# Kernel optimization log

Hardware: AMD Instinct MI355X
Metric: run time of the kernel (lower is better)

Reference implementation:

```python
import jax, jax.numpy as jnp
import numpy as np

# dims
B, N, L = 8, 128, 512          # batch, n_vars, context_window
PL, ST = 16, 8                  # patch_len, stride
PN = (L - PL) // ST + 1         # patch_num = 63
DM, H, DFF, NL = 128, 16, 256, 2
DK = DM // H
DG, MP, BETA = 8, 3, 0.05       # d_gcn, mp_layers, propbeta
TW = 96                         # target_window


def setup_inputs() -> dict:
    key = jax.random.key(0)
    ks = iter(jax.random.split(key, 64))
    def nrm(shape, s=0.02):
        return jax.random.normal(next(ks), shape, jnp.float32) * s
    inp = {
        "x": jax.random.normal(next(ks), (B, N, L), jnp.float32),
        "adj_logits": jax.random.normal(next(ks), (B, L, N, N), jnp.float32),
        # DGCN params
        "dgcn_start_w": nrm((1, DG)), "dgcn_start_b": jnp.zeros((DG,), jnp.float32),
        "dgcn_mlp_w": nrm(((MP + 1) * DG, 1)), "dgcn_mlp_b": jnp.zeros((1,), jnp.float32),
        # patch embedding + positional
        "W_P": nrm((PL, DM)), "b_P": jnp.zeros((DM,), jnp.float32), "W_pos": nrm((PN, DM)),
        # encoder layers (stacked over NL)
        "Wq": nrm((NL, DM, DM)), "bq": jnp.zeros((NL, DM), jnp.float32),
        "Wk": nrm((NL, DM, DM)), "bk": jnp.zeros((NL, DM), jnp.float32),
        "Wv": nrm((NL, DM, DM)), "bv": jnp.zeros((NL, DM), jnp.float32),
        "Wo": nrm((NL, DM, DM)), "bo": jnp.zeros((NL, DM), jnp.float32),
        "scale": jnp.full((NL,), DK ** -0.5, jnp.float32),
        "bn1_g": jnp.ones((NL, DM), jnp.float32), "bn1_b": jnp.zeros((NL, DM), jnp.float32),
        "ff_w1": nrm((NL, DM, DFF)), "ff_b1": jnp.zeros((NL, DFF), jnp.float32),
        "ff_w2": nrm((NL, DFF, DM)), "ff_b2": jnp.zeros((NL, DM), jnp.float32),
        "bn2_g": jnp.ones((NL, DM), jnp.float32), "bn2_b": jnp.zeros((NL, DM), jnp.float32),
        # head
        "head_w": nrm((DM * PN, TW)), "head_b": jnp.zeros((TW,), jnp.float32),
    }
    return inp


def _bn(x, g, b):
    # BatchNorm1d in training mode over (batch, seq) per feature channel
    mu = x.mean(axis=(0, 1))
    var = x.var(axis=(0, 1))
    return (x - mu) * jax.lax.rsqrt(var + 1e-5) * g + b


def reference(x, adj_logits, dgcn_start_w, dgcn_start_b, dgcn_mlp_w, dgcn_mlp_b,
              W_P, b_P, W_pos, Wq, bq, Wk, bk, Wv, bv, Wo, bo, scale,
              bn1_g, bn1_b, ff_w1, ff_b1, ff_w2, ff_b2, bn2_g, bn2_b,
              head_w, head_b):
    # ---- DGCN: multi-hop diffusion over variables, per time step ----
    x4 = x[..., None]                                   # [b,n,s,1]
    A = jax.nn.softmax(adj_logits, axis=2)              # [b,s,n,m], normalized over source n
    a = jnp.transpose(A, (0, 2, 3, 1))                  # [b,n,m,s]
    h = x4 @ dgcn_start_w + dgcn_start_b                # [b,n,s,d_gcn]
    outs = [h]
    for _ in range(MP):
        h = BETA * x4 + (1.0 - BETA) * jnp.einsum('bnsc,bnms->bmsc', h, a)
        outs.append(h)
    y = (jnp.concatenate(outs, axis=-1) @ dgcn_mlp_w + dgcn_mlp_b)[..., 0]  # [b,n,s]
    # ---- patching ----
    win = jnp.arange(PN)[:, None] * ST + jnp.arange(PL)[None, :]
    z = y[:, :, win]                                    # [b,n,pn,pl]
    # ---- TSTiEncoder (channel independent) ----
    src = (z @ W_P + b_P).reshape(B * N, PN, DM) + W_pos
    prev = None
    for l in range(NL):
        q = (src @ Wq[l] + bq[l]).reshape(-1, PN, H, DK).transpose(0, 2, 1, 3)
        k = (src @ Wk[l] + bk[l]).reshape(-1, PN, H, DK).transpose(0, 2, 1, 3)
        v = (src @ Wv[l] + bv[l]).reshape(-1, PN, H, DK).transpose(0, 2, 1, 3)
        scores = jnp.einsum('bhqd,bhkd->bhqk', q, k) * scale[l]
        if prev is not None:
            scores = scores + prev                      # residual attention
        w = jax.nn.softmax(scores, axis=-1)
        o = jnp.einsum('bhqk,bhkd->bhqd', w, v).transpose(0, 2, 1, 3).reshape(-1, PN, DM)
        src = _bn(src + (o @ Wo[l] + bo[l]), bn1_g[l], bn1_b[l])
        ff = jax.nn.gelu(src @ ff_w1[l] + ff_b1[l], approximate=False) @ ff_w2[l] + ff_b2[l]
        src = _bn(src + ff, bn2_g[l], bn2_b[l])
        prev = scores
    # ---- Flatten_Head ----
    enc = src.reshape(B, N, PN, DM).transpose(0, 1, 3, 2).reshape(B, N, DM * PN)
    return enc @ head_w + head_b                        # [b, n_vars, target_window]
```

## Files before the change

### kernel.cpp

```cpp
#include <hip/hip_runtime.h>
#include <hip/hip_bf16.h>
#include <math.h>

#define RM 64512

typedef short short8 __attribute__((ext_vector_type(8)));
typedef float f32x4 __attribute__((ext_vector_type(4)));
typedef unsigned short ushort4v __attribute__((ext_vector_type(4)));
typedef unsigned short ushort8v __attribute__((ext_vector_type(8)));

__device__ __forceinline__ float gelu_f(float v) {
    return 0.5f * v * (1.0f + erff(v * 0.70710678118654752f));
}
__device__ __forceinline__ float b2f(unsigned short u) {
    unsigned int x = ((unsigned int)u) << 16;
    return __builtin_bit_cast(float, x);
}
__device__ __forceinline__ unsigned short f2b(float f) {
    __hip_bfloat16 h = __float2bfloat16(f);
    return __builtin_bit_cast(unsigned short, h);
}

__global__ __launch_bounds__(256) void dgcn_kernel(
    const float* __restrict__ x, const float* __restrict__ adj,
    const float* __restrict__ sw, const float* __restrict__ sb,
    const float* __restrict__ mw, const float* __restrict__ mb,
    float* __restrict__ y,
    const float* __restrict__ Wq, const float* __restrict__ Wk, const float* __restrict__ Wv,
    const float* __restrict__ Wo, const float* __restrict__ fw1, const float* __restrict__ fw2,
    const float* __restrict__ bq, const float* __restrict__ bk, const float* __restrict__ bv,
    unsigned short* __restrict__ WB, float* __restrict__ bcat)
{
    if (blockIdx.x >= 4096) {
        const int wb = blockIdx.x - 4096;
        const int id = wb / 64, bx = wb % 64;
        const int l = id / 6, mat = id % 6;
        const float* src; int K, N; size_t off = (size_t)l * 131072;
        switch (mat) {
            case 0: src = Wq  + l*16384; K = 128; N = 128; off += 0;      break;
            case 1: src = Wk  + l*16384; K = 128; N = 128; off += 16384;  break;
            case 2: src = Wv  + l*16384; K = 128; N = 128; off += 32768;  break;
            case 3: src = Wo  + l*16384; K = 128; N = 128; off += 49152;  break;
            case 4: src = fw1 + l*32768; K = 128; N = 256; off += 65536;  break;
            default:src = fw2 + l*32768; K = 256; N = 128; off += 98304;  break;
        }
        const int total = K * N;
        const int ksh = (K == 256) ? 8 : 7;
        for (int idx = bx*256 + threadIdx.x; idx < total; idx += 64*256) {
            int n = idx >> ksh, k = idx & (K - 1);
            WB[off + idx] = f2b(src[(size_t)k*N + n]);
        }
        if (id == 0 && bx == 0) {
            for (int idx = threadIdx.x; idx < 768; idx += 256) {
                int ll = idx / 384, j = idx % 384;
                float vv;
                if (j < 128)      vv = bq[ll*128 + j];
                else if (j < 256) vv = bk[ll*128 + j - 128];
                else              vv = bv[ll*128 + j - 256];
                bcat[idx] = vv;
            }
        }
        return;
    }
    __shared__ __align__(16) unsigned short ET[128*128];
    __shared__ __align__(16) unsigned short hT[16*128];
    __shared__ float red[256];
    __shared__ float iv[128];
    __shared__ float xc[128];
    __shared__ float yac[128];
    const int bid = blockIdx.x;
    const int b = bid >> 9, s = bid & 511;
    const int t = threadIdx.x;
    const int lane = t & 63, wid = t >> 6;
    const float* ap = adj + (size_t)bid * 16384;

    if (t < 128) xc[t] = x[((size_t)b*128 + t)*512 + s];

    {
        const int m = t & 127, ng = t >> 7;
        float sm = 0.f;
        for (int p = 0; p < 16; ++p) {
            const int n0 = p*8 + ng*4;
            float e0 = __expf(ap[(size_t)(n0+0)*128 + m]);
            float e1 = __expf(ap[(size_t)(n0+1)*128 + m]);
            float e2 = __expf(ap[(size_t)(n0+2)*128 + m]);
            float e3 = __expf(ap[(size_t)(n0+3)*128 + m]);
            sm += e0 + e1 + e2 + e3;
            ushort4v u4; u4[0]=f2b(e0); u4[1]=f2b(e1); u4[2]=f2b(e2); u4[3]=f2b(e3);
            *(ushort4v*)((char*)ET + m*256 + (((n0>>3) ^ (m & 15))*16) + (n0 & 7)*2) = u4;
        }
        red[ng*128 + m] = sm;
        *(ushort4v*)&hT[8*128 + t*4] = (ushort4v){0,0,0,0};
    }
    __syncthreads();
    if (t < 128) iv[t] = 1.f / (red[t] + red[128 + t]);
    if (t < 128) {
        const int m = t;
        const float xm = xc[m];
        float yp = 0.f;
        #pragma unroll
        for (int c = 0; c < 8; ++c) {
            float h = xm*sw[c] + sb[c];
            yp += h*mw[c];
            *(unsigned short*)((char*)hT + c*256 + ((((m>>3) ^ c))*16) + (m & 7)*2) = f2b(h);
        }
        yac[m] = yp;
    }
    __syncthreads();

    const int rl = lane & 15, kh = lane >> 4;
    short8 af[2][4];
    float xr[2][4], ivr[2][4];
    #pragma unroll
    for (int ti = 0; ti < 2; ++ti) {
        const int mrow = (wid*2 + ti)*16 + rl;
        #pragma unroll
        for (int ks = 0; ks < 4; ++ks) {
            const int ch = (ks*4 + kh) ^ (mrow & 15);
            af[ti][ks] = *(const short8*)((const char*)ET + mrow*256 + ch*16);
        }
        #pragma unroll
        for (int r = 0; r < 4; ++r) {
            const int m = (wid*2 + ti)*16 + kh*4 + r;
            xr[ti][r]  = 0.05f * xc[m];
            ivr[ti][r] = 0.95f * iv[m];
        }
    }
    float yl[2][4] = {};
    #pragma unroll
    for (int step = 1; step <= 3; ++step) {
        short8 bfr[4];
        #pragma unroll
        for (int ks = 0; ks < 4; ++ks) {
            const int ch = (ks*4 + kh) ^ rl;
            bfr[ks] = *(const short8*)((const char*)hT + rl*256 + ch*16);
        }
        f32x4 acc[2] = {};
        #pragma unroll
        for (int ti = 0; ti < 2; ++ti)
            #pragma unroll
            for (int ks = 0; ks < 4; ++ks)
                acc[ti] = __builtin_amdgcn_mfma_f32_16x16x32_bf16(af[ti][ks], bfr[ks], acc[ti], 0, 0, 0);
        __syncthreads();
        const float mwc = (rl < 8) ? mw[step*8 + rl] : 0.f;
        #pragma unroll
        for (int ti = 0; ti < 2; ++ti) {
            const int m0 = (wid*2 + ti)*16 + kh*4;
            ushort4v hw4;
            float hnew[4];
            #pragma unroll
            for (int r = 0; r < 4; ++r) {
                float v = xr[ti][r] + ivr[ti][r]*acc[ti][r];
                hnew[r] = v;
                hw4[r] = f2b(v);
            }
            *(ushort4v*)((char*)hT + rl*256 + (((m0>>3) ^ rl)*16) + (m0 & 7)*2) = hw4;
            #pragma unroll
            for (int r = 0; r < 4; ++r) {
                float vv = hnew[r]*mwc;
                vv += __shfl_xor(vv, 1);
                vv += __shfl_xor(vv, 2);
                vv += __shfl_xor(vv, 4);
                vv += __shfl_xor(vv, 8);
                yl[ti][r] += vv;
            }
        }
        __syncthreads();
    }
    if (rl == 0) {
        #pragma unroll
        for (int ti = 0; ti < 2; ++ti)
            #pragma unroll
            for (int r = 0; r < 4; ++r)
                yac[(wid*2 + ti)*16 + kh*4 + r] += yl[ti][r];
    }
    __syncthreads();
    if (t < 128) y[((size_t)b*128 + t)*512 + s] = yac[t] + mb[0];
}

__global__ __launch_bounds__(256) void patch_kernel(
    const float* __restrict__ y, const float* __restrict__ Wp, const float* __restrict__ bp,
    const float* __restrict__ Wpos, unsigned short* __restrict__ srcb)
{
    __shared__ float ys[512];
    __shared__ float wps[16*128];
    const int bn = blockIdx.x;
    const int t = threadIdx.x;
    ys[t]       = y[(size_t)bn*512 + t];
    ys[t + 256] = y[(size_t)bn*512 + t + 256];
    #pragma unroll
    for (int r = 0; r < 8; ++r) wps[t + r*256] = Wp[t + r*256];
    __syncthreads();
    for (int cu = t; cu < 1008; cu += 256) {
        int p = cu >> 4, d0 = (cu & 15) * 8;
        float o[8];
        #pragma unroll
        for (int j = 0; j < 8; ++j) o[j] = bp[d0+j] + Wpos[p*128 + d0 + j];
        #pragma unroll
        for (int tt = 0; tt < 16; ++tt) {
            float a = ys[p*8 + tt];
            #pragma unroll
            for (int j = 0; j < 8; ++j) o[j] += a * wps[tt*128 + d0 + j];
        }
        size_t row = (size_t)bn*63 + p;
        ushort8v u;
        #pragma unroll
        for (int j = 0; j < 8; ++j) u[j] = f2b(o[j]);
        *(ushort8v*)&srcb[row*128 + d0] = u;
    }
}

template<int ACT, int OM, int RESMODE, bool STATS, bool AHM, int NB, int KK>
__global__ __launch_bounds__(256) void mgemm(
    const unsigned short* __restrict__ A, const unsigned short* __restrict__ WB,
    const float* __restrict__ bias, const unsigned short* __restrict__ Rsd,
    const float* __restrict__ snR,
    unsigned short* __restrict__ Cb,
    float* __restrict__ part)
{
    constexpr int NTOT = NB * 128;
    constexpr int kch = KK >> 3;
    constexpr int KT = KK >> 7;
    __shared__ __align__(16) unsigned short AsL[64*128];
    __shared__ __align__(16) unsigned short BsL[128*128];
    __shared__ float sred[4][16][8], qred[4][16][8];
    const int t = threadIdx.x;
    const int lane = t & 63, wid = t >> 6;
    const int wr = wid >> 1, wc = wid & 1;
    const int m0 = blockIdx.x * 64;
    const int kh = lane >> 4, rl = lane & 15;
    const int rq = lane >> 4;
    float sj[8] = {}, qj[8] = {};

    for (int ib = 0; ib < NB; ++ib) {
        f32x4 acc[2][4] = {};
        for (int kt = 0; kt < KT; ++kt) {
            if (ib == 0 || KT > 1) {
                #pragma unroll
                for (int i = 0; i < 4; ++i) {
                    int cid = i*256 + t;
                    const unsigned short* ga;
                    if constexpr (AHM) {
                        int hd2 = cid >> 6, row = cid & 63;
                        ga = A + ((size_t)hd2*RM + (m0+row))*8;
                    } else {
                        int row = cid >> 4, c = cid & 15;
                        int c_g = c ^ (row & 7);
                        ga = A + ((size_t)(m0+row)*kch + kt*16 + c_g)*8;
                    }
                    __builtin_amdgcn_global_load_lds((const unsigned int*)ga,
                        (unsigned int*)&AsL[(i*256 + wid*64)*8], 16, 0, 0);
                }
            }
            #pragma unroll
            for (int i = 0; i < 8; ++i) {
                int cid = i*256 + t;
                int nr = cid >> 4, c = cid & 15;
                const unsigned short* gb = WB + (size_t)ib*128*KK
                    + ((size_t)nr*kch + kt*16 + (c ^ (nr & 7)))*8;
                __builtin_amdgcn_global_load_lds((const unsigned int*)gb,
                    (unsigned int*)&BsL[(i*256 + wid*64)*8], 16, 0, 0);
            }
            __syncthreads();
            #pragma unroll
            for (int ks = 0; ks < 4; ++ks) {
                const int cA = ks*4 + kh;
                short8 af[2], bfr[4];
                #pragma unroll
                for (int i = 0; i < 2; ++i) {
                    int row = wr*32 + i*16 + rl;
                    if constexpr (AHM) af[i] = *(const short8*)&AsL[(cA*64 + row)*8];
                    else               af[i] = *(const short8*)&AsL[row*128 + ((cA ^ (row & 7))*8)];
                }
                #pragma unroll
                for (int j = 0; j < 4; ++j) {
                    int cn = wc*64 + j*16 + rl;
                    bfr[j] = *(const short8*)&BsL[cn*128 + ((cA ^ (cn & 7))*8)];
                }
                #pragma unroll
                for (int i = 0; i < 2; ++i)
                    #pragma unroll
                    for (int j = 0; j < 4; ++j)
                        acc[i][j] = __builtin_amdgcn_mfma_f32_16x16x32_bf16(af[i], bfr[j], acc[i][j], 0, 0, 0);
            }
            __syncthreads();
        }
        #pragma unroll
        for (int j = 0; j < 4; ++j) {
            const int col_l = wc*64 + j*16 + rl;
            const float bs = bias[ib*128 + col_l];
            const int chunk = col_l >> 3, bo2 = (col_l & 7) << 1;
            #pragma unroll
            for (int i = 0; i < 2; ++i) {
                #pragma unroll
                for (int r = 0; r < 4; ++r) {
                    const int row_l = wr*32 + i*16 + rq*4 + r;
                    float v = acc[i][j][r] + bs;
                    if constexpr (ACT == 1) v = gelu_f(v);
                    *(unsigned short*)((char*)BsL + row_l*256 + ((chunk ^ (row_l & 15))<<4) + bo2) = f2b(v);
                }
            }
        }
        __syncthreads();
        if constexpr (OM == 1) {
            #pragma unroll
            for (int it = 0; it < 4; ++it) {
                int cid = it*256 + t;
                int row_l = cid & 63, hd_l = cid >> 6;
                ushort8v u = *(const ushort8v*)((const char*)BsL + row_l*256 + ((hd_l ^ (row_l & 15))<<4));
                *(ushort8v*)&Cb[(((size_t)(ib*16 + hd_l))*RM + m0 + row_l)*8] = u;
            }
        } else {
            #pragma unroll
            for (int it = 0; it < 4; ++it) {
                const int row_l = it*16 + (t >> 4), c = t & 15;
                ushort8v u = *(const ushort8v*)((const char*)BsL + row_l*256 + ((c ^ (row_l & 15))<<4));
                const size_t gbase = (size_t)(m0 + row_l)*NTOT + ib*128 + c*8;
                ushort8v rs = {};
                if constexpr (RESMODE != 0) rs = *(const ushort8v*)&Rsd[gbase];
                ushort8v o8;
                #pragma unroll
                for (int jj = 0; jj < 8; ++jj) {
                    float v = b2f(u[jj]);
                    if constexpr (RESMODE == 1) v += b2f(rs[jj]);
                    if constexpr (RESMODE == 2) v += b2f(rs[jj])*snR[c*8+jj] + snR[128 + c*8 + jj];
                    if constexpr (STATS) { sj[jj] += v; qj[jj] += v*v; }
                    o8[jj] = f2b(v);
                }
                *(ushort8v*)&Cb[gbase] = o8;
            }
        }
        __syncthreads();
    }
    if constexpr (STATS) {
        #pragma unroll
        for (int jj = 0; jj < 8; ++jj) {
            sj[jj] += __shfl_xor(sj[jj], 16); qj[jj] += __shfl_xor(qj[jj], 16);
            sj[jj] += __shfl_xor(sj[jj], 32); qj[jj] += __shfl_xor(qj[jj], 32);
        }
        if ((lane >> 4) == 0) {
            #pragma unroll
            for (int jj = 0; jj < 8; ++jj) {
                sred[wid][lane][jj] = sj[jj];
                qred[wid][lane][jj] = qj[jj];
            }
        }
        __syncthreads();
        if (t < 128) {
            const int c2 = t >> 3, jj = t & 7;
            float s = sred[0][c2][jj] + sred[1][c2][jj] + sred[2][c2][jj] + sred[3][c2][jj];
            float q = qred[0][c2][jj] + qred[1][c2][jj] + qred[2][c2][jj] + qred[3][c2][jj];
            part[(size_t)blockIdx.x*256 + t]       = s;
            part[(size_t)blockIdx.x*256 + 128 + t] = q;
        }
    }
}

__global__ __launch_bounds__(256) void ffused(
    const unsigned short* __restrict__ A, const unsigned short* __restrict__ W1,
    const float* __restrict__ b1, const unsigned short* __restrict__ W2,
    const float* __restrict__ b2, const unsigned short* __restrict__ Rsd,
    const float* __restrict__ snR,
    unsigned short* __restrict__ Cb, float* __restrict__ part)
{
    __shared__ __align__(16) char smem[81920];
    unsigned short* AsL = (unsigned short*)smem;
    unsigned short* BsL = (unsigned short*)(smem + 16384);
    unsigned short* G   = (unsigned short*)(smem + 49152);
    float* sred = (float*)(smem + 49152);
    float* qred = sred + 512;
    const int t = threadIdx.x;
    const int lane = t & 63, wid = t >> 6;
    const int wr = wid >> 1, wc = wid & 1;
    const int m0 = blockIdx.x * 64;
    const int kh = lane >> 4, rl = lane & 15;
    const int rq = lane >> 4;

    #pragma unroll
    for (int i = 0; i < 4; ++i) {
        int cid = i*256 + t;
        int row = cid >> 4, c = cid & 15;
        const unsigned short* ga = A + ((size_t)(m0+row)*16 + (c ^ (row & 7)))*8;
        __builtin_amdgcn_global_load_lds((const unsigned int*)ga,
            (unsigned int*)&AsL[(i*256 + wid*64)*8], 16, 0, 0);
    }
    #pragma unroll
    for (int i = 0; i < 8; ++i) {
        int cid = i*256 + t;
        int nr = cid >> 4, c = cid & 15;
        const unsigned short* gb = W1 + ((size_t)nr*16 + (c ^ (nr & 7)))*8;
        __builtin_amdgcn_global_load_lds((const unsigned int*)gb,
            (unsigned int*)&BsL[(i*256 + wid*64)*8], 16, 0, 0);
    }
    __syncthreads();
    for (int ib = 0; ib < 2; ++ib) {
        f32x4 acc[2][4] = {};
        #pragma unroll
        for (int ks = 0; ks < 4; ++ks) {
            const int cA = ks*4 + kh;
            short8 af[2], bfr[4];
            #pragma unroll
            for (int i = 0; i < 2; ++i) {
                int row = wr*32 + i*16 + rl;
                af[i] = *(const short8*)&AsL[row*128 + ((cA ^ (row & 7))*8)];
            }
            #pragma unroll
            for (int j = 0; j < 4; ++j) {
                int cn = wc*64 + j*16 + rl;
                bfr[j] = *(const short8*)&BsL[cn*128 + ((cA ^ (cn & 7))*8)];
            }
            #pragma unroll
            for (int i = 0; i < 2; ++i)
                #pragma unroll
                for (int j = 0; j < 4; ++j)
                    acc[i][j] = __builtin_amdgcn_mfma_f32_16x16x32_bf16(af[i], bfr[j], acc[i][j], 0, 0, 0);
        }
        __syncthreads();
        if (ib == 0) {
            #pragma unroll
            for (int i = 0; i < 8; ++i) {
                int cid = i*256 + t;
                int nr = cid >> 4, c = cid & 15;
                const unsigned short* gb = W1 + ((size_t)(128+nr)*16 + (c ^ (nr & 7)))*8;
                __builtin_amdgcn_global_load_lds((const unsigned int*)gb,
                    (unsigned int*)&BsL[(i*256 + wid*64)*8], 16, 0, 0);
            }
        }
        #pragma unroll
        for (int j = 0; j < 4; ++j) {
            const int col_l = wc*64 + j*16 + rl;
            const int colg = ib*128 + col_l;
            const float bs = b1[colg];
            const int cg = colg >> 3, bo2 = (colg & 7) << 1;
            #pragma unroll
            for (int i = 0; i < 2; ++i) {
                #pragma unroll
                for (int r = 0; r < 4; ++r) {
                    const int row_l = wr*32 + i*16 + rq*4 + r;
                    float v = gelu_f(acc[i][j][r] + bs);
                    *(unsigned short*)((char*)G + row_l*512 + (((cg ^ (row_l & 15)))<<4) + bo2) = f2b(v);
                }
            }
        }
        __syncthreads();
    }
    f32x4 acc2[2][4] = {};
    for (int kt = 0; kt < 2; ++kt) {
        #pragma unroll
        for (int i = 0; i < 8; ++i) {
            int cid = i*256 + t;
            int nr = cid >> 4, c = cid & 15;
            const unsigned short* gb = W2 + ((size_t)nr*32 + kt*16 + (c ^ (nr & 7)))*8;
            __builtin_amdgcn_global_load_lds((const unsigned int*)gb,
                (unsigned int*)&BsL[(i*256 + wid*64)*8], 16, 0, 0);
        }
        __syncthreads();
        #pragma unroll
        for (int ks = 0; ks < 4; ++ks) {
            const int cA = ks*4 + kh;
            short8 af[2], bfr[4];
            #pragma unroll
            for (int i = 0; i < 2; ++i) {
                int row = wr*32 + i*16 + rl;
                af[i] = *(const short8*)((const char*)G + row*512 + ((((kt*16 + cA) ^ (row & 15)))<<4));
            }
            #pragma unroll
            for (int j = 0; j < 4; ++j) {
                int cn = wc*64 + j*16 + rl;
                bfr[j] = *(const short8*)&BsL[cn*128 + ((cA ^ (cn & 7))*8)];
            }
            #pragma unroll
            for (int i = 0; i < 2; ++i)
                #pragma unroll
                for (int j = 0; j < 4; ++j)
                    acc2[i][j] = __builtin_amdgcn_mfma_f32_16x16x32_bf16(af[i], bfr[j], acc2[i][j], 0, 0, 0);
        }
        __syncthreads();
    }
    #pragma unroll
    for (int j = 0; j < 4; ++j) {
        const int col_l = wc*64 + j*16 + rl;
        const float bs = b2[col_l];
        const int chunk = col_l >> 3, bo2 = (col_l & 7) << 1;
        #pragma unroll
        for (int i = 0; i < 2; ++i) {
            #pragma unroll
            for (int r = 0; r < 4; ++r) {
                const int row_l = wr*32 + i*16 + rq*4 + r;
                *(unsigned short*)((char*)AsL + row_l*256 + ((chunk ^ (row_l & 15))<<4) + bo2)
                    = f2b(acc2[i][j][r] + bs);
            }
        }
    }
    __syncthreads();
    float sj[8] = {}, qj[8] = {};
    #pragma unroll
    for (int it = 0; it < 4; ++it) {
        const int row_l = it*16 + (t >> 4), c = t & 15;
        ushort8v u = *(const ushort8v*)((const char*)AsL + row_l*256 + ((c ^ (row_l & 15))<<4));
        const size_t gbase = (size_t)(m0 + row_l)*128 + c*8;
        ushort8v rs = *(const ushort8v*)&Rsd[gbase];
        ushort8v o8;
        #pragma unroll
        for (int jj = 0; jj < 8; ++jj) {
            float v = b2f(u[jj]) + b2f(rs[jj])*snR[c*8+jj] + snR[128 + c*8 + jj];
            sj[jj] += v; qj[jj] += v*v;
            o8[jj] = f2b(v);
        }
        *(ushort8v*)&Cb[gbase] = o8;
    }
    #pragma unroll
    for (int jj = 0; jj < 8; ++jj) {
        sj[jj] += __shfl_xor(sj[jj], 16); qj[jj] += __shfl_xor(qj[jj], 16);
        sj[jj] += __shfl_xor(sj[jj], 32); qj[jj] += __shfl_xor(qj[jj], 32);
    }
    if ((lane >> 4) == 0) {
        #pragma unroll
        for (int jj = 0; jj < 8; ++jj) {
            sred[wid*128 + lane*8 + jj] = sj[jj];
            qred[wid*128 + lane*8 + jj] = qj[jj];
        }
    }
    __syncthreads();
    if (t < 128) {
        const int c2 = t >> 3, jj = t & 7;
        float s = sred[0*128 + c2*8 + jj] + sred[1*128 + c2*8 + jj]
                + sred[2*128 + c2*8 + jj] + sred[3*128 + c2*8 + jj];
        float q = qred[0*128 + c2*8 + jj] + qred[1*128 + c2*8 + jj]
                + qred[2*128 + c2*8 + jj] + qred[3*128 + c2*8 + jj];
        part[(size_t)blockIdx.x*256 + t]       = s;
        part[(size_t)blockIdx.x*256 + 128 + t] = q;
    }
}

__global__ __launch_bounds__(256) void bnred(const float* __restrict__ part,
    const float* __restrict__ g, const float* __restrict__ b, float* __restrict__ sn)
{
    const int c = blockIdx.x, t = threadIdx.x;
    float s = 0.f, q = 0.f;
    for (int bid = t; bid < 1008; bid += 256) {
        s += part[(size_t)bid*256 + c];
        q += part[(size_t)bid*256 + 128 + c];
    }
    __shared__ float ls[256], lq[256];
    ls[t] = s; lq[t] = q;
    __syncthreads();
    for (int o = 128; o > 0; o >>= 1) {
        if (t < o) { ls[t] += ls[t+o]; lq[t] += lq[t+o]; }
        __syncthreads();
    }
    if (t == 0) {
        const float invM = 1.f / (float)RM;
        float mean = ls[0] * invM;
        float var  = fmaxf(lq[0]*invM - mean*mean, 0.f);
        float sc = g[c] * rsqrtf(var + 1e-5f);
        sn[c]       = sc;
        sn[128 + c] = b[c] - mean*sc;
    }
}

__global__ __launch_bounds__(256) void wfold(const unsigned short* __restrict__ WBs,
    const float* __restrict__ sn, const float* __restrict__ bsrc,
    unsigned short* __restrict__ WBd, float* __restrict__ bdst)
{
    const int t = threadIdx.x, wv = t >> 6, lane = t & 63;
    const int n = blockIdx.x*4 + wv;
    float w1 = b2f(WBs[(size_t)n*128 + lane]);
    float w2 = b2f(WBs[(size_t)n*128 + 64 + lane]);
    WBd[(size_t)n*128 + lane]      = f2b(sn[lane]*w1);
    WBd[(size_t)n*128 + 64 + lane] = f2b(sn[64+lane]*w2);
    float bacc = sn[128+lane]*w1 + sn[192+lane]*w2;
    #pragma unroll
    for (int msk = 1; msk < 64; msk <<= 1) bacc += __shfl_xor(bacc, msk);
    if (lane == 0) bdst[n] = bsrc[n] + bacc;
}

template<int L>
__global__ __launch_bounds__(256) void attn_kernel(
    const unsigned short* __restrict__ qkv, const unsigned short* __restrict__ qkvP,
    const float* __restrict__ scale, unsigned short* __restrict__ ob)
{
    __shared__ float ks[4][504], vs[4][504], k0s[4][504];
    const int bn = blockIdx.x;
    const int t = threadIdx.x, wid = t >> 6, lane = t & 63;
    const int hd = blockIdx.y*4 + wid;
    const size_t rbase = (size_t)hd*RM + (size_t)bn*63;
    float qr[8] = {}, q0r[8] = {};
    if (lane < 63) {
        ushort8v ku = *(const ushort8v*)&qkv[((size_t)16*RM*8) + (rbase + lane)*8];
        ushort8v vu = *(const ushort8v*)&qkv[((size_t)32*RM*8) + (rbase + lane)*8];
        #pragma unroll
        for (int d = 0; d < 8; ++d) { ks[wid][lane*8+d] = b2f(ku[d]); vs[wid][lane*8+d] = b2f(vu[d]); }
        ushort8v qu = *(const ushort8v*)&qkv[(rbase + lane)*8];
        #pragma unroll
        for (int d = 0; d < 8; ++d) qr[d] = b2f(qu[d]);
        if constexpr (L > 0) {
            ushort8v k0u = *(const ushort8v*)&qkvP[((size_t)16*RM*8) + (rbase + lane)*8];
            #pragma unroll
            for (int d = 0; d < 8; ++d) k0s[wid][lane*8+d] = b2f(k0u[d]);
            ushort8v q0u = *(const ushort8v*)&qkvP[(rbase + lane)*8];
            #pragma unroll
            for (int d = 0; d < 8; ++d) q0r[d] = b2f(q0u[d]);
        }
    }
    __syncthreads();
    if (lane >= 63) return;
    const float scl  = scale[L];
    const float scl0 = (L > 0) ? scale[0] : 0.f;
    float sum = 0.f;
    float oa[8] = {};
    for (int j = 0; j < 63; ++j) {
        float s = 0.f;
        #pragma unroll
        for (int d = 0; d < 8; ++d) s += qr[d]*ks[wid][j*8+d];
        s *= scl;
        if constexpr (L > 0) {
            float s0 = 0.f;
            #pragma unroll
            for (int d = 0; d < 8; ++d) s0 += q0r[d]*k0s[wid][j*8+d];
            s += scl0 * s0;
        }
        float p = __expf(s);
        sum += p;
        #pragma unroll
        for (int d = 0; d < 8; ++d) oa[d] += p*vs[wid][j*8+d];
    }
    float inv = 1.f / sum;
    ushort8v u;
    #pragma unroll
    for (int d = 0; d < 8; ++d) u[d] = f2b(oa[d]*inv);
    *(ushort8v*)&ob[((size_t)hd*RM + (size_t)bn*63 + lane)*8] = u;
}

__global__ __launch_bounds__(256) void hprep(
    const float* __restrict__ hw, const float* __restrict__ hb,
    const float* __restrict__ sn,
    unsigned short* __restrict__ hwTf, float* __restrict__ hbf)
{
    const int t = threadIdx.x;
    if (blockIdx.x < 63) {
        const int p = blockIdx.x;
        for (int idx = t; idx < 16384; idx += 256) {
            int n = idx >> 7, d = idx & 127;
            unsigned short w = 0;
            if (n < 96) w = f2b(sn[d] * hw[(size_t)(d*63 + p)*96 + n]);
            hwTf[((size_t)p*128 + n)*128 + d] = w;
        }
    } else {
        const int n = blockIdx.x - 63;
        float acc = 0.f;
        for (int k = t; k < 8064; k += 256) {
            int d = (int)(((unsigned)k * 33289u) >> 21);
            acc += sn[128 + d] * hw[(size_t)k*96 + n];
        }
        __shared__ float ls[256];
        ls[t] = acc;
        __syncthreads();
        for (int o = 128; o > 0; o >>= 1) { if (t < o) ls[t] += ls[t+o]; __syncthreads(); }
        if (t == 0) hbf[n] = hb[n] + ls[0];
    }
}

__global__ __launch_bounds__(256) void mhead(
    const unsigned short* __restrict__ A, const unsigned short* __restrict__ BW,
    float* __restrict__ part)
{
    __shared__ __align__(16) unsigned short AsL[128*128];
    __shared__ __align__(16) unsigned short BsL[128*128];
    const int t = threadIdx.x;
    const int lane = t & 63, wid = t >> 6;
    const int wr = wid >> 1, wc = wid & 1;
    const int m0 = blockIdx.x * 128;
    const int p  = blockIdx.y;
    #pragma unroll
    for (int i = 0; i < 8; ++i) {
        int cid = i*256 + t;
        int row = cid >> 4, c = cid & 15;
        const unsigned short* ga = A + ((size_t)(m0+row)*63 + p)*128 + ((c ^ (row & 7))*8);
        __builtin_amdgcn_global_load_lds((const unsigned int*)ga,
            (unsigned int*)&AsL[(i*256 + wid*64)*8], 16, 0, 0);
    }
    #pragma unroll
    for (int i = 0; i < 8; ++i) {
        int cid = i*256 + t;
        int nr = cid >> 4, c = cid & 15;
        const unsigned short* gb = BW + ((size_t)p*128 + nr)*128 + ((c ^ (nr & 7))*8);
        __builtin_amdgcn_global_load_lds((const unsigned int*)gb,
            (unsigned int*)&BsL[(i*256 + wid*64)*8], 16, 0, 0);
    }
    __syncthreads();
    const int kh = lane >> 4, rl = lane & 15;
    f32x4 acc[4][3] = {};
    #pragma unroll
    for (int kq = 0; kq < 4; ++kq) {
        const int cA = kq*4 + kh;
        short8 af[4], bfr[3];
        #pragma unroll
        for (int i = 0; i < 4; ++i) {
            int row = wr*64 + i*16 + rl;
            af[i] = *(const short8*)&AsL[row*128 + ((cA ^ (row & 7))*8)];
        }
        #pragma unroll
        for (int j = 0; j < 3; ++j) {
            int cn = wc*48 + j*16 + rl;
            bfr[j] = *(const short8*)&BsL[cn*128 + ((cA ^ (cn & 7))*8)];
        }
        #pragma unroll
        for (int i = 0; i < 4; ++i)
            #pragma unroll
            for (int j = 0; j < 3; ++j)
                acc[i][j] = __builtin_amdgcn_mfma_f32_16x16x32_bf16(af[i], bfr[j], acc[i][j], 0, 0, 0);
    }
    const int rl2 = lane & 15, rq = lane >> 4;
    #pragma unroll
    for (int j = 0; j < 3; ++j) {
        const int col = wc*48 + j*16 + rl2;
        #pragma unroll
        for (int i = 0; i < 4; ++i) {
            const int rbase = m0 + wr*64 + i*16 + rq*4;
            #pragma unroll
            for (int r = 0; r < 4; ++r)
                part[((size_t)p*1024 + rbase + r)*96 + col] = acc[i][j][r];
        }
    }
}

__global__ __launch_bounds__(256) void head_reduce(const float* __restrict__ part,
    const float* __restrict__ hbf, float* __restrict__ out)
{
    int idx = blockIdx.x*256 + threadIdx.x;
    float s = hbf[idx % 96];
    #pragma unroll
    for (int blk = 0; blk < 63; ++blk) s += part[(size_t)blk*98304 + idx];
    out[idx] = s;
}

extern "C" void kernel_launch(void* const* d_in, const int* in_sizes, int n_in,
                              void* d_out, int out_size, void* d_ws, size_t ws_size,
                              hipStream_t stream) {
    const float* x    = (const float*)d_in[0];
    const float* adj  = (const float*)d_in[1];
    const float* sw   = (const float*)d_in[2];
    const float* sb   = (const float*)d_in[3];
    const float* mw   = (const float*)d_in[4];
    const float* mb   = (const float*)d_in[5];
    const float* Wp   = (const float*)d_in[6];
    const float* bp   = (const float*)d_in[7];
    const float* Wpos = (const float*)d_in[8];
    const float* Wq   = (const float*)d_in[9];
    const float* bq   = (const float*)d_in[10];
    const float* Wk   = (const float*)d_in[11];
    const float* bk   = (const float*)d_in[12];
    const float* Wv   = (const float*)d_in[13];
    const float* bv   = (const float*)d_in[14];
    const float* Wo   = (const float*)d_in[15];
    const float* bo   = (const float*)d_in[16];
    const float* scale= (const float*)d_in[17];
    const float* bn1g = (const float*)d_in[18];
    const float* bn1b = (const float*)d_in[19];
    const float* fw1  = (const float*)d_in[20];
    const float* fb1  = (const float*)d_in[21];
    const float* fw2  = (const float*)d_in[22];
    const float* fb2  = (const float*)d_in[23];
    const float* bn2g = (const float*)d_in[24];
    const float* bn2b = (const float*)d_in[25];
    const float* hw   = (const float*)d_in[26];
    const float* hb   = (const float*)d_in[27];
    float* out = (float*)d_out;

    float* y     = (float*)d_ws;
    float* part  = y     + 524288;
    float* snorm = part  + 258048;
    float* bcat  = snorm + 1024;
    float* bfold = bcat  + 768;
    float* hbf   = bfold + 1024;
    float* hpart = hbf   + 128;
    unsigned short* srcb = (unsigned short*)(hpart + 6193152);
    unsigned short* t1b  = srcb + 8257536;
    unsigned short* t2b  = t1b  + 8257536;
    unsigned short* g    = t2b  + 8257536;
    unsigned short* o_bf = g    + 16515072;
    unsigned short* qkv0 = o_bf + 8257536;
    unsigned short* qkv1 = qkv0 + 24772608;
    unsigned short* WB   = qkv1 + 24772608;
    unsigned short* WF   = WB   + 262144;
    unsigned short* hwTf = WF   + 131072;

    dgcn_kernel<<<4864, 256, 0, stream>>>(x, adj, sw, sb, mw, mb, y,
        Wq, Wk, Wv, Wo, fw1, fw2, bq, bk, bv, WB, bcat);
    patch_kernel<<<1024, 256, 0, stream>>>(y, Wp, bp, Wpos, srcb);

    mgemm<0,1,0,false,false,3,128><<<1008, 256, 0, stream>>>(srcb, WB, bcat, nullptr, nullptr, qkv0, nullptr);
    attn_kernel<0><<<dim3(1024,4), 256, 0, stream>>>(qkv0, qkv0, scale, o_bf);
    mgemm<0,2,1,true,true,1,128><<<1008, 256, 0, stream>>>(o_bf, WB + 49152, bo, srcb, nullptr, t1b, part);
    bnred<<<128, 256, 0, stream>>>(part, bn1g, bn1b, snorm);
    wfold<<<64, 256, 0, stream>>>(WB + 65536, snorm, fb1, WF, bfold);
    ffused<<<1008, 256, 0, stream>>>(t1b, WF, bfold, WB + 98304, fb2, t1b, snorm, t2b, part);
    bnred<<<128, 256, 0, stream>>>(part, bn2g, bn2b, snorm + 256);
    wfold<<<96, 256, 0, stream>>>(WB + 131072, snorm + 256, bcat + 384, WF + 65536, bfold + 512);

    mgemm<0,1,0,false,false,3,128><<<1008, 256, 0, stream>>>(t2b, WF + 65536, bfold + 512, nullptr, nullptr, qkv1, nullptr);
    attn_kernel<1><<<dim3(1024,4), 256, 0, stream>>>(qkv1, qkv0, scale, o_bf);
    mgemm<0,2,2,true,true,1,128><<<1008, 256, 0, stream>>>(o_bf, WB + 131072 + 49152, bo + 128, t2b, snorm + 256, t1b, part);
    bnred<<<128, 256, 0, stream>>>(part, bn1g + 128, bn1b + 128, snorm + 512);
    wfold<<<64, 256, 0, stream>>>(WB + 131072 + 65536, snorm + 512, fb1 + 256, WF + 32768, bfold + 256);
    ffused<<<1008, 256, 0, stream>>>(t1b, WF + 32768, bfold + 256, WB + 131072 + 98304, fb2 + 128, t1b, snorm + 512, t2b, part);
    bnred<<<128, 256, 0, stream>>>(part, bn2g + 128, bn2b + 128, snorm + 768);

    hprep<<<159, 256, 0, stream>>>(hw, hb, snorm + 768, hwTf, hbf);
    mhead<<<dim3(8,63), 256, 0, stream>>>(t2b, hwTf, hpart);
    head_reduce<<<384, 256, 0, stream>>>(hpart, hbf, out);
}
```

Measured before the change: 373.1 us.

## Fuse QKV projection GEMM with attention per patch sequence

```diff
diff --git a/kernel.cpp b/kernel.cpp
--- a/kernel.cpp
+++ b/kernel.cpp
@@ -356,6 +356,125 @@
     }
 }
 
+template<int L>
+__global__ __launch_bounds__(256) void qkattn(
+    const unsigned short* __restrict__ A, const unsigned short* __restrict__ WBq,
+    const float* __restrict__ bias, const float* __restrict__ scale,
+    const unsigned short* __restrict__ q0k0, unsigned short* __restrict__ q0k0out,
+    unsigned short* __restrict__ ob)
+{
+    __shared__ __align__(16) char smem[81920];
+    unsigned short* AsL = (unsigned short*)smem;
+    unsigned short* BsL = (unsigned short*)(smem + 16384);
+    unsigned short* QKV = (unsigned short*)(smem + 32768);
+    const int t = threadIdx.x;
+    const int lane = t & 63, wid = t >> 6;
+    const int bn = blockIdx.x;
+    const size_t r0 = (size_t)bn * 63;
+    const int kh = lane >> 4, rl = lane & 15, rq = lane >> 4;
+
+    #pragma unroll
+    for (int i = 0; i < 4; ++i) {
+        int cid = i*256 + t;
+        int row = cid >> 4, c = cid & 15;
+        size_t gr = r0 + row; if (gr >= RM) gr = RM - 1;
+        const unsigned short* ga = A + (gr*16 + (size_t)(c ^ (row & 7)))*8;
+        __builtin_amdgcn_global_load_lds((const unsigned int*)ga,
+            (unsigned int*)&AsL[(i*256 + wid*64)*8], 16, 0, 0);
+    }
+    for (int c6 = 0; c6 < 6; ++c6) {
+        #pragma unroll
+        for (int i = 0; i < 4; ++i) {
+            int cid = i*256 + t;
+            int nr = cid >> 4, c = cid & 15;
+            const unsigned short* gb = WBq + ((size_t)(c6*64 + nr)*16 + (c ^ (nr & 7)))*8;
+            __builtin_amdgcn_global_load_lds((const unsigned int*)gb,
+                (unsigned int*)&BsL[(i*256 + wid*64)*8], 16, 0, 0);
+        }
+        __syncthreads();
+        f32x4 acc[4] = {};
+        #pragma unroll
+        for (int ks = 0; ks < 4; ++ks) {
+            const int cA = ks*4 + kh;
+            const int cn = wid*16 + rl;
+            short8 bfr = *(const short8*)&BsL[cn*128 + ((cA ^ (cn & 7))*8)];
+            #pragma unroll
+            for (int i = 0; i < 4; ++i) {
+                int row = i*16 + rl;
+                short8 af = *(const short8*)&AsL[row*128 + ((cA ^ (row & 7))*8)];
+                acc[i] = __builtin_amdgcn_mfma_f32_16x16x32_bf16(af, bfr, acc[i], 0, 0, 0);
+            }
+        }
+        __syncthreads();
+        const int col = c6*64 + wid*16 + rl;
+        const int hd = col >> 3, d = col & 7;
+        const float bs = bias[col];
+        #pragma unroll
+        for (int i = 0; i < 4; ++i)
+            #pragma unroll
+            for (int r = 0; r < 4; ++r) {
+                int row = i*16 + rq*4 + r;
+                QKV[(size_t)(hd*64 + row)*8 + d] = f2b(acc[i][r] + bs);
+            }
+    }
+    if constexpr (L > 0) {
+        for (int idx = t; idx < 16*63; idx += 256) {
+            int hd2 = idx / 63, j = idx - hd2*63;
+            ushort8v u = *(const ushort8v*)&q0k0[(((size_t)(16 + hd2))*RM + r0 + j)*8];
+            *(ushort8v*)&BsL[(hd2*63 + j)*8] = u;
+        }
+    }
+    __syncthreads();
+    if constexpr (L == 0) {
+        for (int idx = t; idx < 32*63; idx += 256) {
+            int hd2 = idx / 63, j = idx - hd2*63;
+            ushort8v u = *(const ushort8v*)&QKV[(size_t)(hd2*64 + j)*8];
+            *(ushort8v*)&q0k0out[((size_t)hd2*RM + r0 + j)*8] = u;
+        }
+    }
+    if (lane >= 63) return;
+    const float scl  = scale[L];
+    const float scl0 = (L > 0) ? scale[0] : 0.f;
+    for (int hh = 0; hh < 4; ++hh) {
+        const int hd = wid*4 + hh;
+        float qr[8], q0r[8] = {};
+        ushort8v qu = *(const ushort8v*)&QKV[(size_t)(hd*64 + lane)*8];
+        #pragma unroll
+        for (int d = 0; d < 8; ++d) qr[d] = b2f(qu[d]);
+        if constexpr (L > 0) {
+            ushort8v q0u = *(const ushort8v*)&q0k0[((size_t)hd*RM + r0 + lane)*8];
+            #pragma unroll
+            for (int d = 0; d < 8; ++d) q0r[d] = b2f(q0u[d]);
+        }
+        float sum = 0.f;
+        float oa[8] = {};
+        for (int j = 0; j < 63; ++j) {
+            ushort8v ku = *(const ushort8v*)&QKV[(size_t)((16 + hd)*64 + j)*8];
+            float s = 0.f;
+            #pragma unroll
+            for (int d = 0; d < 8; ++d) s += qr[d]*b2f(ku[d]);
+            s *= scl;
+            if constexpr (L > 0) {
+                ushort8v k0u = *(const ushort8v*)&BsL[(hd*63 + j)*8];
+                float s0 = 0.f;
+                #pragma unroll
+                for (int d = 0; d < 8; ++d) s0 += q0r[d]*b2f(k0u[d]);
+                s += scl0 * s0;
+            }
+            float p = __expf(s);
+            sum += p;
+            ushort8v vu = *(const ushort8v*)&QKV[(size_t)((32 + hd)*64 + j)*8];
+            #pragma unroll
+            for (int d = 0; d < 8; ++d) oa[d] += p*b2f(vu[d]);
+        }
+        float inv = 1.f / sum;
+        ushort8v u;
+        #pragma unroll
+        for (int d = 0; d < 8; ++d) u[d] = f2b(oa[d]*inv);
+        *(ushort8v*)&ob[((size_t)hd*RM + r0 + lane)*8] = u;
+    }
+}
+
 __global__ __launch_bounds__(256) void ffused(
     const unsigned short* __restrict__ A, const unsigned short* __restrict__ W1,
     const float* __restrict__ b1, const unsigned short* __restrict__ W2,
@@ -573,63 +692,6 @@
     #pragma unroll
     for (int msk = 1; msk < 64; msk <<= 1) bacc += __shfl_xor(bacc, msk);
     if (lane == 0) bdst[n] = bsrc[n] + bacc;
-}
-
-template<int L>
-__global__ __launch_bounds__(256) void attn_kernel(
-    const unsigned short* __restrict__ qkv, const unsigned short* __restrict__ qkvP,
-    const float* __restrict__ scale, unsigned short* __restrict__ ob)
-{
-    __shared__ float ks[4][504], vs[4][504], k0s[4][504];
-    const int bn = blockIdx.x;
-    const int t = threadIdx.x, wid = t >> 6, lane = t & 63;
-    const int hd = blockIdx.y*4 + wid;
-    const size_t rbase = (size_t)hd*RM + (size_t)bn*63;
-    float qr[8] = {}, q0r[8] = {};
-    if (lane < 63) {
-        ushort8v ku = *(const ushort8v*)&qkv[((size_t)16*RM*8) + (rbase + lane)*8];
-        ushort8v vu = *(const ushort8v*)&qkv[((size_t)32*RM*8) + (rbase + lane)*8];
-        #pragma unroll
-        for (int d = 0; d < 8; ++d) { ks[wid][lane*8+d] = b2f(ku[d]); vs[wid][lane*8+d] = b2f(vu[d]); }
-        ushort8v qu = *(const ushort8v*)&qkv[(rbase + lane)*8];
-        #pragma unroll
-        for (int d = 0; d < 8; ++d) qr[d] = b2f(qu[d]);
-        if constexpr (L > 0) {
-            ushort8v k0u = *(const ushort8v*)&qkvP[((size_t)16*RM*8) + (rbase + lane)*8];
-            #pragma unroll
-            for (int d = 0; d < 8; ++d) k0s[wid][lane*8+d] = b2f(k0u[d]);
-            ushort8v q0u = *(const ushort8v*)&qkvP[(rbase + lane)*8];
-            #pragma unroll
-            for (int d = 0; d < 8; ++d) q0r[d] = b2f(q0u[d]);
-        }
-    }
-    __syncthreads();
-    if (lane >= 63) return;
-    const float scl  = scale[L];
-    const float scl0 = (L > 0) ? scale[0] : 0.f;
-    float sum = 0.f;
-    float oa[8] = {};
-    for (int j = 0; j < 63; ++j) {
-        float s = 0.f;
-        #pragma unroll
-        for (int d = 0; d < 8; ++d) s += qr[d]*ks[wid][j*8+d];
-        s *= scl;
-        if constexpr (L > 0) {
-            float s0 = 0.f;
-            #pragma unroll
-            for (int d = 0; d < 8; ++d) s0 += q0r[d]*k0s[wid][j*8+d];
-            s += scl0 * s0;
-        }
-        float p = __expf(s);
-        sum += p;
-        #pragma unroll
-        for (int d = 0; d < 8; ++d) oa[d] += p*vs[wid][j*8+d];
-    }
-    float inv = 1.f / sum;
-    ushort8v u;
-    #pragma unroll
-    for (int d = 0; d < 8; ++d) u[d] = f2b(oa[d]*inv);
-    *(ushort8v*)&ob[((size_t)hd*RM + (size_t)bn*63 + lane)*8] = u;
 }
 
 __global__ __launch_bounds__(256) void hprep(
@@ -778,11 +840,9 @@
     unsigned short* srcb = (unsigned short*)(hpart + 6193152);
     unsigned short* t1b  = srcb + 8257536;
     unsigned short* t2b  = t1b  + 8257536;
-    unsigned short* g    = t2b  + 8257536;
-    unsigned short* o_bf = g    + 16515072;
-    unsigned short* qkv0 = o_bf + 8257536;
-    unsigned short* qkv1 = qkv0 + 24772608;
-    unsigned short* WB   = qkv1 + 24772608;
+    unsigned short* o_bf = t2b  + 8257536;
+    unsigned short* q0k0 = o_bf + 8257536;
+    unsigned short* WB   = q0k0 + 16515072;
     unsigned short* WF   = WB   + 262144;
     unsigned short* hwTf = WF   + 131072;
 
@@ -790,8 +850,7 @@
         Wq, Wk, Wv, Wo, fw1, fw2, bq, bk, bv, WB, bcat);
     patch_kernel<<<1024, 256, 0, stream>>>(y, Wp, bp, Wpos, srcb);
 
-    mgemm<0,1,0,false,false,3,128><<<1008, 256, 0, stream>>>(srcb, WB, bcat, nullptr, nullptr, qkv0, nullptr);
-    attn_kernel<0><<<dim3(1024,4), 256, 0, stream>>>(qkv0, qkv0, scale, o_bf);
+    qkattn<0><<<1024, 256, 0, stream>>>(srcb, WB, bcat, scale, nullptr, q0k0, o_bf);
     mgemm<0,2,1,true,true,1,128><<<1008, 256, 0, stream>>>(o_bf, WB + 49152, bo, srcb, nullptr, t1b, part);
     bnred<<<128, 256, 0, stream>>>(part, bn1g, bn1b, snorm);
     wfold<<<64, 256, 0, stream>>>(WB + 65536, snorm, fb1, WF, bfold);
@@ -799,8 +858,7 @@
     bnred<<<128, 256, 0, stream>>>(part, bn2g, bn2b, snorm + 256);
     wfold<<<96, 256, 0, stream>>>(WB + 131072, snorm + 256, bcat + 384, WF + 65536, bfold + 512);
 
-    mgemm<0,1,0,false,false,3,128><<<1008, 256, 0, stream>>>(t2b, WF + 65536, bfold + 512, nullptr, nullptr, qkv1, nullptr);
-    attn_kernel<1><<<dim3(1024,4), 256, 0, stream>>>(qkv1, qkv0, scale, o_bf);
+    qkattn<1><<<1024, 256, 0, stream>>>(t2b, WF + 65536, bfold + 512, scale, q0k0, nullptr, o_bf);
     mgemm<0,2,2,true,true,1,128><<<1008, 256, 0, stream>>>(o_bf, WB + 131072 + 49152, bo + 128, t2b, snorm + 256, t1b, part);
     bnred<<<128, 256, 0, stream>>>(part, bn1g + 128, bn1b + 128, snorm + 512);
     wfold<<<64, 256, 0, stream>>>(WB + 131072 + 65536, snorm + 512, fb1 + 256, WF + 32768, bfold + 256);
```

After: 437.5 us. +17.3%, slower.
